# Kernel optimization log

Measured on AMD Instinct MI355X. Metric: run time of the kernel, lower is better.

## Reference

```python
import jax, jax.numpy as jnp
import numpy as np

INPUT_SIZE = 1024
HIDDEN_SIZE = 1024
BATCH = 16384


def setup_inputs() -> dict:
    key = jax.random.key(0)
    kx, kh, kw, kb = jax.random.split(key, 4)
    x = jax.random.normal(kx, (BATCH, INPUT_SIZE), dtype=jnp.float32)
    hidden = jax.random.normal(kh, (BATCH, HIDDEN_SIZE), dtype=jnp.float32)
    fan_in = INPUT_SIZE + HIDDEN_SIZE
    bound = 1.0 / np.sqrt(fan_in)
    # torch Linear: weight [out, in], bias [out], uniform(-bound, bound)
    W = jax.random.uniform(kw, (HIDDEN_SIZE, fan_in), minval=-bound, maxval=bound, dtype=jnp.float32)
    b = jax.random.uniform(kb, (HIDDEN_SIZE,), minval=-bound, maxval=bound, dtype=jnp.float32)
    return {"x": x, "hidden": hidden, "W": W, "b": b}


def reference(x, hidden, W, b):
    # Batched equivalent of the per-sample loop: concat features, linear, tanh.
    xh = jnp.concatenate([x, hidden], axis=1)            # [B, in+hid]
    return jnp.tanh(xh @ W.T + b)                        # [B, hid]
```

## Files before the change

kernel.cpp:

```cpp
#include <hip/hip_runtime.h>
#include <hip/hip_bf16.h>


typedef __bf16 bf16_t;
typedef __bf16 bf16x8 __attribute__((ext_vector_type(8)));
typedef float  f32x4  __attribute__((ext_vector_type(4)));

#define M_GLOBAL 16384
#define N_GLOBAL 1024
#define K_GLOBAL 2048
#define IN_STRIDE 1024

__device__ __forceinline__ float fast_tanh(float v) {
    float e = __expf(2.0f * v);
    return 1.0f - 2.0f * __builtin_amdgcn_rcpf(e + 1.0f);
}

#define XH_UNITS ((long long)M_GLOBAL * K_GLOBAL / 8)
#define W_UNITS  ((long long)N_GLOBAL * K_GLOBAL / 8)

__global__ __launch_bounds__(256)
void cvt_pass(const float* __restrict__ x, const float* __restrict__ h,
              const float* __restrict__ W,
              bf16_t* __restrict__ XHb, bf16_t* __restrict__ Wb)
{
    const long long total = XH_UNITS + W_UNITS;
    for (long long u = (long long)blockIdx.x * 256 + threadIdx.x; u < total;
         u += (long long)gridDim.x * 256) {
        const float* src;
        bf16_t* dst;
        if (u < XH_UNITS) {
            const long long e = u * 8;
            const int row = (int)(e >> 11);
            const int col = (int)(e & 2047);
            src = (col < 1024) ? (x + (long long)row * IN_STRIDE + col)
                               : (h + (long long)row * IN_STRIDE + (col - 1024));
            dst = XHb + e;
        } else {
            const long long e = (u - XH_UNITS) * 8;
            src = W + e;
            dst = Wb + e;
        }
        const float4 v0 = *(const float4*)src;
        const float4 v1 = *(const float4*)(src + 4);
        bf16x8 o;
        o[0] = (bf16_t)v0.x; o[1] = (bf16_t)v0.y;
        o[2] = (bf16_t)v0.z; o[3] = (bf16_t)v0.w;
        o[4] = (bf16_t)v1.x; o[5] = (bf16_t)v1.y;
        o[6] = (bf16_t)v1.z; o[7] = (bf16_t)v1.w;
        *(bf16x8*)dst = o;
    }
}

#define NT 32

__device__ __forceinline__ void gload_lds16(const bf16_t* g, bf16_t* l) {
    __builtin_amdgcn_global_load_lds(
        (const __attribute__((address_space(1))) void*)g,
        (__attribute__((address_space(3))) void*)l, 16, 0, 0);
}

__global__ __launch_bounds__(512, 2)
void gemm8p(const bf16_t* __restrict__ XHb, const bf16_t* __restrict__ Wb,
            const float* __restrict__ bias, float* __restrict__ out)
{
    __shared__ __align__(16) bf16_t lds[2 * 32768];

    const int tid = threadIdx.x;
    const int xcd  = blockIdx.x & 7;
    const int lid  = xcd * 32 + (blockIdx.x >> 3);
    const int bm   = (lid & 63) * 256;
    const int bn   = (lid >> 6) * 256;

    const int lane = tid & 63;
    const int wid  = tid >> 6;
    const int wm = wid >> 2;
    const int wn = wid & 3;
    const int lr = lane & 15;
    const int lk = lane >> 4;
    const int s7 = lr & 7;

    const int srow = lane >> 3;
    const int scol = ((lane & 7) ^ srow) * 8;
    const int c0   = wid * 2;
    const bf16_t* aS = XHb + (size_t)(bm + c0 * 8 + srow) * K_GLOBAL + scol;
    const bf16_t* bS = Wb  + (size_t)(bn + c0 * 8 + srow) * K_GLOBAL + scol;

    const int aRd = wm * 8192 + lr * 64;
    const int bRd = (2 + (wn >> 1)) * 8192 + ((wn & 1) * 64 + lr) * 64;
    const int sl0 = ((0 + lk) ^ s7) * 8;
    const int sl1 = ((4 + lk) ^ s7) * 8;

    f32x4 acc[8][4];
#pragma unroll
    for (int i = 0; i < 8; ++i)
#pragma unroll
        for (int j = 0; j < 4; ++j)
            acc[i][j] = (f32x4){0.f, 0.f, 0.f, 0.f};

#define STAGE(D, PART, T) {                                                   \
    const bf16_t* g_ = (((PART) < 2) ? aS : bS)                               \
        + (size_t)(((PART) & 1) * 128) * K_GLOBAL + (T) * 64;                 \
    bf16_t* l_ = lds + (D) * 32768 + (PART) * 8192 + c0 * 512;                \
    gload_lds16(g_, l_);                                                      \
    gload_lds16(g_ + (size_t)8 * K_GLOBAL, l_ + 512);                         \
}

#define BAR() { asm volatile("" ::: "memory");                                \
                __builtin_amdgcn_s_barrier();                                 \
                asm volatile("" ::: "memory"); }
#define VM4() asm volatile("s_waitcnt vmcnt(4)" ::: "memory")
#define VM0() asm volatile("s_waitcnt vmcnt(0)" ::: "memory")

#define PHASE(DB, M0, FIRSTK, ...) {                                          \
    const int dbo_ = (DB) * 32768;                                            \
    if (FIRSTK) {                                                             \
        _Pragma("unroll")                                                     \
        for (int nf_ = 0; nf_ < 4; ++nf_) {                                   \
            br[nf_][0] = *(const bf16x8*)(lds + dbo_ + bRd + nf_ * 1024 + sl0); \
            br[nf_][1] = *(const bf16x8*)(lds + dbo_ + bRd + nf_ * 1024 + sl1); \
        }                                                                     \
    }                                                                         \
    bf16x8 a00_ = *(const bf16x8*)(lds + dbo_ + aRd + (M0) * 1024 + sl0);     \
    bf16x8 a01_ = *(const bf16x8*)(lds + dbo_ + aRd + (M0) * 1024 + sl1);     \
    bf16x8 a10_ = *(const bf16x8*)(lds + dbo_ + aRd + ((M0) + 1) * 1024 + sl0); \
    bf16x8 a11_ = *(const bf16x8*)(lds + dbo_ + aRd + ((M0) + 1) * 1024 + sl1); \
    __VA_ARGS__;                                                              \
    asm volatile("" ::: "memory");                                            \
    __builtin_amdgcn_s_barrier();                                             \
    asm volatile("s_waitcnt lgkmcnt(0)" ::: "memory");                        \
    __builtin_amdgcn_sched_barrier(0);                                        \
    __builtin_amdgcn_s_setprio(1);                                            \
    _Pragma("unroll")                                                         \
    for (int nf_ = 0; nf_ < 4; ++nf_) {                                       \
        acc[M0][nf_] = __builtin_amdgcn_mfma_f32_16x16x32_bf16(               \
            a00_, br[nf_][0], acc[M0][nf_], 0, 0, 0);                         \
        acc[M0][nf_] = __builtin_amdgcn_mfma_f32_16x16x32_bf16(               \
            a01_, br[nf_][1], acc[M0][nf_], 0, 0, 0);                         \
        acc[(M0) + 1][nf_] = __builtin_amdgcn_mfma_f32_16x16x32_bf16(         \
            a10_, br[nf_][0], acc[(M0) + 1][nf_], 0, 0, 0);                   \
        acc[(M0) + 1][nf_] = __builtin_amdgcn_mfma_f32_16x16x32_bf16(         \
            a11_, br[nf_][1], acc[(M0) + 1][nf_], 0, 0, 0);                   \
    }                                                                         \
    __builtin_amdgcn_s_setprio(0);                                            \
}

    bf16x8 br[4][2];

    STAGE(0, 0, 0); STAGE(0, 1, 0); STAGE(0, 2, 0); STAGE(0, 3, 0);
    STAGE(1, 2, 1); STAGE(1, 3, 1);
    VM4();
    BAR();

    for (int i = 0; i < 15; ++i) {
        const int T1 = 2 * i + 1, T2 = 2 * i + 2, T3 = 2 * i + 3;
        PHASE(0, 0, 1, STAGE(1, 0, T1));        BAR();
        PHASE(0, 2, 0, STAGE(1, 1, T1));        BAR();
        PHASE(0, 4, 0, STAGE(0, 2, T2));        BAR();
        PHASE(0, 6, 0, STAGE(0, 3, T2)); VM4(); BAR();
        PHASE(1, 0, 1, STAGE(0, 0, T2));        BAR();
        PHASE(1, 2, 0, STAGE(0, 1, T2));        BAR();
        PHASE(1, 4, 0, STAGE(1, 2, T3));        BAR();
        PHASE(1, 6, 0, STAGE(1, 3, T3)); VM4(); BAR();
    }
    PHASE(0, 0, 1, STAGE(1, 0, 31));        BAR();
    PHASE(0, 2, 0, STAGE(1, 1, 31));        BAR();
    PHASE(0, 4, 0, );                        BAR();
    PHASE(0, 6, 0, ); VM0();                 BAR();
    PHASE(1, 0, 1, );                        BAR();
    PHASE(1, 2, 0, );                        BAR();
    PHASE(1, 4, 0, );                        BAR();
    PHASE(1, 6, 0, );

#undef PHASE
#undef STAGE
#undef BAR
#undef VM4
#undef VM0

    float bv[4];
#pragma unroll
    for (int nf = 0; nf < 4; ++nf)
        bv[nf] = bias[bn + wn * 64 + nf * 16 + lr];
#pragma unroll
    for (int mf = 0; mf < 8; ++mf) {
#pragma unroll
        for (int nf = 0; nf < 4; ++nf) {
            const int col = bn + wn * 64 + nf * 16 + lr;
#pragma unroll
            for (int r = 0; r < 4; ++r) {
                const int row = bm + wm * 128 + mf * 16 + lk * 4 + r;
                out[(size_t)row * N_GLOBAL + col] = fast_tanh(acc[mf][nf][r] + bv[nf]);
            }
        }
    }
}

#define FNT 32
__global__ __launch_bounds__(256, 2)
void rnncell_fused(const float* __restrict__ x, const float* __restrict__ h,
                   const float* __restrict__ W, const float* __restrict__ bias,
                   float* __restrict__ out)
{
    __shared__ __align__(16) bf16_t As[2][128 * 64];
    __shared__ __align__(16) bf16_t Bs[2][128 * 64];

    const int tid = threadIdx.x;
    const int bid = blockIdx.x;
    const int bm = (bid >> 3) * 128;
    const int bn = (bid & 7) * 128;

    const int lane = tid & 63;
    const int wid  = tid >> 6;
    const int wr = (wid >> 1) * 64;
    const int wc = (wid & 1) * 64;
    const int lr = lane & 15;
    const int lk = lane >> 4;

    const int row0 = tid >> 3;
    const int sl0  = tid & 7;

    f32x4 acc[4][4];
#pragma unroll
    for (int i = 0; i < 4; ++i)
#pragma unroll
        for (int j = 0; j < 4; ++j)
            acc[i][j] = (f32x4){0.f, 0.f, 0.f, 0.f};

    float4 la[4][2], lb[4][2];

#define F_LOAD_A(T) do {                                                      \
    const int k0_ = (T) * 64;                                                 \
    const float* sA_ = (k0_ < 1024)                                           \
        ? (x + (size_t)bm * IN_STRIDE + k0_)                                  \
        : (h + (size_t)bm * IN_STRIDE + (k0_ - 1024));                        \
    _Pragma("unroll")                                                         \
    for (int i_ = 0; i_ < 4; ++i_) {                                          \
        const float* pa_ = sA_ + (size_t)(row0 + i_ * 32) * IN_STRIDE + sl0 * 8; \
        la[i_][0] = *(const float4*)(pa_);                                    \
        la[i_][1] = *(const float4*)(pa_ + 4);                                \
    }                                                                         \
} while (0)

#define F_LOAD_B(T) do {                                                      \
    const float* sB_ = W + (size_t)bn * K_GLOBAL + (T) * 64;                  \
    _Pragma("unroll")                                                         \
    for (int i_ = 0; i_ < 4; ++i_) {                                          \
        const float* pb_ = sB_ + (size_t)(row0 + i_ * 32) * K_GLOBAL + sl0 * 8; \
        lb[i_][0] = *(const float4*)(pb_);                                    \
        lb[i_][1] = *(const float4*)(pb_ + 4);                                \
    }                                                                         \
} while (0)

    F_LOAD_A(0);
    F_LOAD_B(0);

    for (int t = 0; t < FNT; ++t) {
        bf16_t* __restrict__ Ab = As[t & 1];
        bf16_t* __restrict__ Bb = Bs[t & 1];

#pragma unroll
        for (int i = 0; i < 4; ++i) {
            const int row = row0 + i * 32;
            const int ssl = sl0 ^ (row & 7);
            bf16x8 va;
            va[0] = (bf16_t)la[i][0].x; va[1] = (bf16_t)la[i][0].y;
            va[2] = (bf16_t)la[i][0].z; va[3] = (bf16_t)la[i][0].w;
            va[4] = (bf16_t)la[i][1].x; va[5] = (bf16_t)la[i][1].y;
            va[6] = (bf16_t)la[i][1].z; va[7] = (bf16_t)la[i][1].w;
            *(bf16x8*)(Ab + row * 64 + ssl * 8) = va;
        }
#pragma unroll
        for (int i = 0; i < 4; ++i) {
            const int row = row0 + i * 32;
            const int ssl = sl0 ^ (row & 7);
            bf16x8 vb;
            vb[0] = (bf16_t)lb[i][0].x; vb[1] = (bf16_t)lb[i][0].y;
            vb[2] = (bf16_t)lb[i][0].z; vb[3] = (bf16_t)lb[i][0].w;
            vb[4] = (bf16_t)lb[i][1].x; vb[5] = (bf16_t)lb[i][1].y;
            vb[6] = (bf16_t)lb[i][1].z; vb[7] = (bf16_t)lb[i][1].w;
            *(bf16x8*)(Bb + row * 64 + ssl * 8) = vb;
        }

        __syncthreads();

        if (t + 1 < FNT) F_LOAD_A(t + 1);

#pragma unroll
        for (int kk = 0; kk < 2; ++kk) {
            bf16x8 af[4], bfr[4];
#pragma unroll
            for (int mf = 0; mf < 4; ++mf) {
                const int row = wr + mf * 16 + lr;
                const int sl  = (kk * 4 + lk) ^ (row & 7);
                af[mf] = *(const bf16x8*)(Ab + row * 64 + sl * 8);
            }
#pragma unroll
            for (int nf = 0; nf < 4; ++nf) {
                const int row = wc + nf * 16 + lr;
                const int sl  = (kk * 4 + lk) ^ (row & 7);
                bfr[nf] = *(const bf16x8*)(Bb + row * 64 + sl * 8);
            }
#pragma unroll
            for (int mf = 0; mf < 4; ++mf)
#pragma unroll
                for (int nf = 0; nf < 4; ++nf)
                    acc[mf][nf] = __builtin_amdgcn_mfma_f32_16x16x32_bf16(
                        af[mf], bfr[nf], acc[mf][nf], 0, 0, 0);
        }

        if (t + 1 < FNT) F_LOAD_B(t + 1);
    }
#undef F_LOAD_A
#undef F_LOAD_B

    float bv[4];
#pragma unroll
    for (int nf = 0; nf < 4; ++nf)
        bv[nf] = bias[bn + wc + nf * 16 + lr];
#pragma unroll
    for (int mf = 0; mf < 4; ++mf) {
#pragma unroll
        for (int nf = 0; nf < 4; ++nf) {
            const int col = bn + wc + nf * 16 + lr;
#pragma unroll
            for (int r = 0; r < 4; ++r) {
                const int row = bm + wr + mf * 16 + lk * 4 + r;
                out[(size_t)row * N_GLOBAL + col] = fast_tanh(acc[mf][nf][r] + bv[nf]);
            }
        }
    }
}

extern "C" void kernel_launch(void* const* d_in, const int* in_sizes, int n_in,
                              void* d_out, int out_size, void* d_ws, size_t ws_size,
                              hipStream_t stream) {
    (void)in_sizes; (void)n_in; (void)out_size;
    const float* x = (const float*)d_in[0];
    const float* h = (const float*)d_in[1];
    const float* W = (const float*)d_in[2];
    const float* b = (const float*)d_in[3];
    float* out = (float*)d_out;

    const size_t need = ((size_t)M_GLOBAL + N_GLOBAL) * K_GLOBAL * sizeof(bf16_t);
    if (ws_size >= need) {
        bf16_t* XHb = (bf16_t*)d_ws;
        bf16_t* Wb  = XHb + (size_t)M_GLOBAL * K_GLOBAL;
        cvt_pass<<<2048, 256, 0, stream>>>(x, h, W, XHb, Wb);
        gemm8p<<<256, 512, 0, stream>>>(XHb, Wb, b, out);
    } else {
        rnncell_fused<<<1024, 256, 0, stream>>>(x, h, W, b, out);
    }
}
```

Baseline: 101.3 us.

## Split phases by K-half with 4 M-fragments and reschedule LDS staging

```diff
diff --git a/kernel.cpp b/kernel.cpp
--- a/kernel.cpp
+++ b/kernel.cpp
@@ -10,6 +10,7 @@
 #define N_GLOBAL 1024
 #define K_GLOBAL 2048
 #define IN_STRIDE 1024
+#define NT 32
 
 __device__ __forceinline__ float fast_tanh(float v) {
     float e = __expf(2.0f * v);
@@ -52,8 +53,6 @@
     }
 }
 
-#define NT 32
-
 __device__ __forceinline__ void gload_lds16(const bf16_t* g, bf16_t* l) {
     __builtin_amdgcn_global_load_lds(
         (const __attribute__((address_space(1))) void*)g,
@@ -88,8 +87,6 @@
 
     const int aRd = wm * 8192 + lr * 64;
     const int bRd = (2 + (wn >> 1)) * 8192 + ((wn & 1) * 64 + lr) * 64;
-    const int sl0 = ((0 + lk) ^ s7) * 8;
-    const int sl1 = ((4 + lk) ^ s7) * 8;
 
     f32x4 acc[8][4];
 #pragma unroll
@@ -109,22 +106,21 @@
 #define BAR() { asm volatile("" ::: "memory");                                \
                 __builtin_amdgcn_s_barrier();                                 \
                 asm volatile("" ::: "memory"); }
-#define VM4() asm volatile("s_waitcnt vmcnt(4)" ::: "memory")
+#define VM2() asm volatile("s_waitcnt vmcnt(2)" ::: "memory")
 #define VM0() asm volatile("s_waitcnt vmcnt(0)" ::: "memory")
 
-#define PHASE(DB, M0, FIRSTK, ...) {                                          \
+#define PHASE(DB, SLK, M0, READB, ...) {                                      \
     const int dbo_ = (DB) * 32768;                                            \
-    if (FIRSTK) {                                                             \
+    const int sl_  = (((SLK) + lk) ^ s7) * 8;                                 \
+    if (READB) {                                                              \
         _Pragma("unroll")                                                     \
-        for (int nf_ = 0; nf_ < 4; ++nf_) {                                   \
-            br[nf_][0] = *(const bf16x8*)(lds + dbo_ + bRd + nf_ * 1024 + sl0); \
-            br[nf_][1] = *(const bf16x8*)(lds + dbo_ + bRd + nf_ * 1024 + sl1); \
-        }                                                                     \
+        for (int nf_ = 0; nf_ < 4; ++nf_)                                     \
+            bq[nf_] = *(const bf16x8*)(lds + dbo_ + bRd + nf_ * 1024 + sl_);  \
     }                                                                         \
-    bf16x8 a00_ = *(const bf16x8*)(lds + dbo_ + aRd + (M0) * 1024 + sl0);     \
-    bf16x8 a01_ = *(const bf16x8*)(lds + dbo_ + aRd + (M0) * 1024 + sl1);     \
-    bf16x8 a10_ = *(const bf16x8*)(lds + dbo_ + aRd + ((M0) + 1) * 1024 + sl0); \
-    bf16x8 a11_ = *(const bf16x8*)(lds + dbo_ + aRd + ((M0) + 1) * 1024 + sl1); \
+    bf16x8 a0_ = *(const bf16x8*)(lds + dbo_ + aRd + ((M0) + 0) * 1024 + sl_); \
+    bf16x8 a1_ = *(const bf16x8*)(lds + dbo_ + aRd + ((M0) + 1) * 1024 + sl_); \
+    bf16x8 a2_ = *(const bf16x8*)(lds + dbo_ + aRd + ((M0) + 2) * 1024 + sl_); \
+    bf16x8 a3_ = *(const bf16x8*)(lds + dbo_ + aRd + ((M0) + 3) * 1024 + sl_); \
     __VA_ARGS__;                                                              \
     asm volatile("" ::: "memory");                                            \
     __builtin_amdgcn_s_barrier();                                             \
@@ -133,49 +129,49 @@
     __builtin_amdgcn_s_setprio(1);                                            \
     _Pragma("unroll")                                                         \
     for (int nf_ = 0; nf_ < 4; ++nf_) {                                       \
-        acc[M0][nf_] = __builtin_amdgcn_mfma_f32_16x16x32_bf16(               \
-            a00_, br[nf_][0], acc[M0][nf_], 0, 0, 0);                         \
-        acc[M0][nf_] = __builtin_amdgcn_mfma_f32_16x16x32_bf16(               \
-            a01_, br[nf_][1], acc[M0][nf_], 0, 0, 0);                         \
+        acc[(M0) + 0][nf_] = __builtin_amdgcn_mfma_f32_16x16x32_bf16(         \
+            a0_, bq[nf_], acc[(M0) + 0][nf_], 0, 0, 0);                       \
         acc[(M0) + 1][nf_] = __builtin_amdgcn_mfma_f32_16x16x32_bf16(         \
-            a10_, br[nf_][0], acc[(M0) + 1][nf_], 0, 0, 0);                   \
-        acc[(M0) + 1][nf_] = __builtin_amdgcn_mfma_f32_16x16x32_bf16(         \
-            a11_, br[nf_][1], acc[(M0) + 1][nf_], 0, 0, 0);                   \
+            a1_, bq[nf_], acc[(M0) + 1][nf_], 0, 0, 0);                       \
+        acc[(M0) + 2][nf_] = __builtin_amdgcn_mfma_f32_16x16x32_bf16(         \
+            a2_, bq[nf_], acc[(M0) + 2][nf_], 0, 0, 0);                       \
+        acc[(M0) + 3][nf_] = __builtin_amdgcn_mfma_f32_16x16x32_bf16(         \
+            a3_, bq[nf_], acc[(M0) + 3][nf_], 0, 0, 0);                       \
     }                                                                         \
     __builtin_amdgcn_s_setprio(0);                                            \
 }
 
-    bf16x8 br[4][2];
+    bf16x8 bq[4];
 
     STAGE(0, 0, 0); STAGE(0, 1, 0); STAGE(0, 2, 0); STAGE(0, 3, 0);
-    STAGE(1, 2, 1); STAGE(1, 3, 1);
-    VM4();
+    STAGE(1, 2, 1);
+    VM2();
     BAR();
 
     for (int i = 0; i < 15; ++i) {
         const int T1 = 2 * i + 1, T2 = 2 * i + 2, T3 = 2 * i + 3;
-        PHASE(0, 0, 1, STAGE(1, 0, T1));        BAR();
-        PHASE(0, 2, 0, STAGE(1, 1, T1));        BAR();
-        PHASE(0, 4, 0, STAGE(0, 2, T2));        BAR();
-        PHASE(0, 6, 0, STAGE(0, 3, T2)); VM4(); BAR();
-        PHASE(1, 0, 1, STAGE(0, 0, T2));        BAR();
-        PHASE(1, 2, 0, STAGE(0, 1, T2));        BAR();
-        PHASE(1, 4, 0, STAGE(1, 2, T3));        BAR();
-        PHASE(1, 6, 0, STAGE(1, 3, T3)); VM4(); BAR();
-    }
-    PHASE(0, 0, 1, STAGE(1, 0, 31));        BAR();
-    PHASE(0, 2, 0, STAGE(1, 1, 31));        BAR();
-    PHASE(0, 4, 0, );                        BAR();
-    PHASE(0, 6, 0, ); VM0();                 BAR();
-    PHASE(1, 0, 1, );                        BAR();
-    PHASE(1, 2, 0, );                        BAR();
-    PHASE(1, 4, 0, );                        BAR();
-    PHASE(1, 6, 0, );
+        PHASE(0, 0, 0, 1, STAGE(1, 0, T1); STAGE(1, 3, T1));  BAR();
+        PHASE(0, 0, 4, 0, STAGE(1, 1, T1));                   BAR();
+        PHASE(0, 4, 0, 1, );                                  BAR();
+        PHASE(0, 4, 4, 0, STAGE(0, 2, T2));            VM2(); BAR();
+        PHASE(1, 0, 0, 1, STAGE(0, 3, T2));                   BAR();
+        PHASE(1, 0, 4, 0, STAGE(0, 0, T2));                   BAR();
+        PHASE(1, 4, 0, 1, STAGE(0, 1, T2));                   BAR();
+        PHASE(1, 4, 4, 0, STAGE(1, 2, T3));            VM2(); BAR();
+    }
+    PHASE(0, 0, 0, 1, STAGE(1, 0, 31); STAGE(1, 3, 31));  BAR();
+    PHASE(0, 0, 4, 0, STAGE(1, 1, 31));                   BAR();
+    PHASE(0, 4, 0, 1, );                                  BAR();
+    PHASE(0, 4, 4, 0, );                           VM0(); BAR();
+    PHASE(1, 0, 0, 1, );                                  BAR();
+    PHASE(1, 0, 4, 0, );                                  BAR();
+    PHASE(1, 4, 0, 1, );                                  BAR();
+    PHASE(1, 4, 4, 0, );
 
 #undef PHASE
 #undef STAGE
 #undef BAR
-#undef VM4
+#undef VM2
 #undef VM0
 
     float bv[4];
```

Measured after the change: 102.6 us. Within noise of the previous version (+1.3%).
